# Kernel optimization log

Measured on AMD Instinct MI355X. Metric: run time of the kernel, lower is better.

The kernel has to match this reference:

```python
import jax, jax.numpy as jnp
import numpy as np

B, S, D, H = 2, 2048, 1024, 16
HD = D // H


def setup_inputs() -> dict:
    key = jax.random.key(0)
    ks = jax.random.split(key, 5)
    scale = 1.0 / np.sqrt(D)
    return {
        "query": jax.random.normal(ks[0], (B, S, D), jnp.float32),
        "Wq": jax.random.normal(ks[1], (D, D), jnp.float32) * scale,
        "bq": jnp.zeros((D,), jnp.float32),
        "Wk": jax.random.normal(ks[2], (D, D), jnp.float32) * scale,
        "bk": jnp.zeros((D,), jnp.float32),
        "Wv": jax.random.normal(ks[3], (D, D), jnp.float32) * scale,
        "bv": jnp.zeros((D,), jnp.float32),
        "Wo": jax.random.normal(ks[4], (D, D), jnp.float32) * scale,
        "bo": jnp.zeros((D,), jnp.float32),
    }


def _split_heads(x):
    # [B, S, D] -> [B, H, S, HD]
    return x.reshape(B, S, H, HD).transpose(0, 2, 1, 3)


def reference(query, Wq, bq, Wk, bk, Wv, bv, Wo, bo):
    # Linear projections (torch Linear: x @ W.T + b)
    q = _split_heads(query @ Wq.T + bq)
    k = _split_heads(query @ Wk.T + bk)  # key defaults to query
    v = _split_heads(query @ Wv.T + bv)  # value defaults to query

    # scaled dot-product attention, scores [B, H, S, S]
    scores = jnp.einsum("bhqd,bhkd->bhqk", q, k) / jnp.sqrt(jnp.float32(HD))
    attn = jax.nn.softmax(scores, axis=-1)
    ctx = jnp.einsum("bhqk,bhkd->bhqd", attn, v)

    # combine heads -> [B, S, D]
    ctx = ctx.transpose(0, 2, 1, 3).reshape(B, S, D)
    out = ctx @ Wo.T + bo
    avg_attn = attn.mean(axis=1)  # [B, S, S]
    return out, avg_attn
```

## Files before the change

kernel.cpp:

```cpp
#include <hip/hip_runtime.h>
#include <hip/hip_bf16.h>

#define BB 2
#define SS 2048
#define DD 1024
#define HH 16
#define HDD 64

typedef __bf16 bf16;
typedef bf16 bf16x8 __attribute__((ext_vector_type(8)));
typedef bf16 bf16x4 __attribute__((ext_vector_type(4)));
typedef float f32x4 __attribute__((ext_vector_type(4)));

typedef const __attribute__((address_space(1))) void* gptr_t;
typedef __attribute__((address_space(3))) void* lptr_t;
#define GLL(gp, lp) __builtin_amdgcn_global_load_lds((gptr_t)(gp), (lptr_t)(lp), 16, 0, 0)

__global__ void cast_bf16_k(const float* __restrict__ src, bf16* __restrict__ dst, int n) {
    int i = (blockIdx.x * blockDim.x + threadIdx.x) * 4;
    if (i < n) {
        const float4 f = *(const float4*)(src + i);
        bf16x4 o;
        o[0] = (bf16)f.x; o[1] = (bf16)f.y; o[2] = (bf16)f.z; o[3] = (bf16)f.w;
        *(bf16x4*)(dst + i) = o;
    }
}

template<int MODE>
__global__ __launch_bounds__(256) void gemm_bt(
    const bf16* __restrict__ A, const bf16* __restrict__ Wbase,
    const float* __restrict__ bias0, const float* __restrict__ bias1,
    const float* __restrict__ bias2, void* __restrict__ outp)
{
    __shared__ alignas(16) bf16 As[2][128 * 32];
    __shared__ alignas(16) bf16 Bs[2][128 * 32];

    const int tid  = threadIdx.x;
    const int lane = tid & 63;
    const int wave = tid >> 6;
    const int wr = wave >> 1, wc = wave & 1;
    const int l15 = lane & 15, g = lane >> 4;
    const int m0 = blockIdx.x * 128, n0 = blockIdx.y * 128;
    const int z = blockIdx.z;
    const bf16* W = Wbase + (size_t)z * (DD * DD);
    const float* bias = (MODE == 0) ? (z == 0 ? bias0 : (z == 1 ? bias1 : bias2)) : bias0;

    const int sr = lane >> 2, sc = (lane & 3) * 8;

#define STAGE(buf, kt) {                                                              \
        const int k0 = (kt) * 32;                                                     \
        _Pragma("unroll")                                                             \
        for (int i = 0; i < 2; ++i) {                                                 \
            const int c = wave * 2 + i;                                               \
            GLL(A + (size_t)(m0 + c * 16 + sr) * DD + k0 + sc, &As[buf][c * 512]);    \
            GLL(W + (size_t)(n0 + c * 16 + sr) * DD + k0 + sc, &Bs[buf][c * 512]);    \
        }                                                                             \
    }

    f32x4 acc[4][4];
#pragma unroll
    for (int mi = 0; mi < 4; ++mi)
#pragma unroll
        for (int ni = 0; ni < 4; ++ni) acc[mi][ni] = f32x4{0.f, 0.f, 0.f, 0.f};

    STAGE(0, 0);
    int cur = 0;
    for (int kt = 0; kt < 32; ++kt) {
        __syncthreads();
        if (kt + 1 < 32) STAGE(cur ^ 1, kt + 1);
        bf16x8 af[4], bfr[4];
#pragma unroll
        for (int mi = 0; mi < 4; ++mi)
            af[mi] = *(const bf16x8*)&As[cur][(wr * 64 + mi * 16 + l15) * 32 + g * 8];
#pragma unroll
        for (int ni = 0; ni < 4; ++ni)
            bfr[ni] = *(const bf16x8*)&Bs[cur][(wc * 64 + ni * 16 + l15) * 32 + g * 8];
#pragma unroll
        for (int mi = 0; mi < 4; ++mi)
#pragma unroll
            for (int ni = 0; ni < 4; ++ni)
                acc[mi][ni] = __builtin_amdgcn_mfma_f32_16x16x32_bf16(af[mi], bfr[ni], acc[mi][ni], 0, 0, 0);
        cur ^= 1;
    }
#undef STAGE

    if (MODE == 0) {
        bf16* obase = (bf16*)outp + (size_t)z * (BB * HH * SS * HDD);
#pragma unroll
        for (int mi = 0; mi < 4; ++mi)
#pragma unroll
            for (int ni = 0; ni < 4; ++ni)
#pragma unroll
                for (int r = 0; r < 4; ++r) {
                    const int grow = m0 + wr * 64 + mi * 16 + g * 4 + r;
                    const int gcol = n0 + wc * 64 + ni * 16 + l15;
                    const float val = acc[mi][ni][r] + bias[gcol];
                    const int b = grow >> 11, s = grow & (SS - 1);
                    const int h = gcol >> 6, hd = gcol & 63;
                    obase[((size_t)(b * HH + h) * SS + s) * HDD + hd] = (bf16)val;
                }
    } else {
        float* obase = (float*)outp;
#pragma unroll
        for (int mi = 0; mi < 4; ++mi)
#pragma unroll
            for (int ni = 0; ni < 4; ++ni)
#pragma unroll
                for (int r = 0; r < 4; ++r) {
                    const int grow = m0 + wr * 64 + mi * 16 + g * 4 + r;
                    const int gcol = n0 + wc * 64 + ni * 16 + l15;
                    obase[(size_t)grow * DD + gcol] = acc[mi][ni][r] + bias[gcol];
                }
    }
}

__global__ __launch_bounds__(256) void transpose_v_k(const bf16* __restrict__ src, bf16* __restrict__ dst)
{
    __shared__ bf16 t[64][72];
    const int tid = threadIdx.x;
    const int s0 = blockIdx.x * 64, bh = blockIdx.y;
    {
        const int r = tid >> 3, c8 = (tid & 7) * 8;
#pragma unroll
        for (int i = 0; i < 2; ++i) {
            const bf16x8 v = *(const bf16x8*)(src + ((size_t)bh * SS + s0 + r + i * 32) * HDD + c8);
#pragma unroll
            for (int j = 0; j < 8; ++j) t[c8 + j][r + i * 32] = v[j];
        }
    }
    __syncthreads();
    {
        const int hd = tid >> 2, sl = (tid & 3) * 2;
#pragma unroll
        for (int i = 0; i < 2; ++i) {
            const bf16x8 o = *(const bf16x8*)&t[hd][(sl + i) * 8];
            *(bf16x8*)(dst + ((size_t)bh * HDD + hd) * SS + s0 + (sl + i) * 8) = o;
        }
    }
}

__global__ __launch_bounds__(512) void attn_flash(
    const bf16* __restrict__ q, const bf16* __restrict__ k, const bf16* __restrict__ vT,
    bf16* __restrict__ ctx, float* __restrict__ lrow)
{
    __shared__ alignas(16) bf16 Kt[2][64 * 64];
    __shared__ alignas(16) bf16 Vt[2][64 * 64];
    __shared__ alignas(16) bf16 Pl[8][16 * 72];

    const int tid = threadIdx.x, lane = tid & 63, wave = tid >> 6;
    const int qt = blockIdx.x, bh = blockIdx.y;
    const int q0 = qt * 128 + wave * 16;
    const size_t base = (size_t)bh * SS * HDD;
    const int l15 = lane & 15, g = lane >> 4;

    const bf16* qp = q + base + (size_t)(q0 + l15) * HDD + g * 8;
    const bf16x8 aq0 = *(const bf16x8*)(qp);
    const bf16x8 aq1 = *(const bf16x8*)(qp + 32);

    const int srow_off = lane >> 3, spos = lane & 7;

#define STAGEKV(buf, kv0) {                                                           \
        const int row = wave * 8 + srow_off;                                          \
        const int gs = spos ^ (row & 7);                                              \
        GLL(k  + base + (size_t)((kv0) + row) * HDD + gs * 8, &Kt[buf][wave * 512]);  \
        GLL(vT + base + (size_t)row * SS + (kv0) + gs * 8,    &Vt[buf][wave * 512]);  \
    }

    f32x4 acc[4];
#pragma unroll
    for (int n = 0; n < 4; ++n) acc[n] = f32x4{0.f, 0.f, 0.f, 0.f};
    float lpart[4] = {0.f, 0.f, 0.f, 0.f};

    STAGEKV(0, 0);
    int cur = 0;
    for (int t = 0; t < 32; ++t) {
        __syncthreads();
        if (t + 1 < 32) STAGEKV(cur ^ 1, (t + 1) * 64);

        f32x4 sc[4];
        __builtin_amdgcn_s_setprio(1);
#pragma unroll
        for (int nn = 0; nn < 4; ++nn) {
            const int row = nn * 16 + l15, rx = row & 7;
            const bf16x8 kf0 = *(const bf16x8*)&Kt[cur][row * 64 + ((g    ) ^ rx) * 8];
            const bf16x8 kf1 = *(const bf16x8*)&Kt[cur][row * 64 + ((4 + g) ^ rx) * 8];
            f32x4 c = f32x4{0.f, 0.f, 0.f, 0.f};
            c = __builtin_amdgcn_mfma_f32_16x16x32_bf16(aq0, kf0, c, 0, 0, 0);
            c = __builtin_amdgcn_mfma_f32_16x16x32_bf16(aq1, kf1, c, 0, 0, 0);
            sc[nn] = c * 0.125f;
        }
        __builtin_amdgcn_s_setprio(0);

#pragma unroll
        for (int nn = 0; nn < 4; ++nn)
#pragma unroll
            for (int r = 0; r < 4; ++r) {
                const float p = __expf(sc[nn][r]);
                lpart[r] += p;
                Pl[wave][(g * 4 + r) * 72 + nn * 16 + l15] = (bf16)p;
            }

        const bf16x8 pa0 = *(const bf16x8*)&Pl[wave][l15 * 72 + g * 8];
        const bf16x8 pa1 = *(const bf16x8*)&Pl[wave][l15 * 72 + 32 + g * 8];
        __builtin_amdgcn_s_setprio(1);
#pragma unroll
        for (int n = 0; n < 4; ++n) {
            const int row = n * 16 + l15, rx = row & 7;
            const bf16x8 vf0 = *(const bf16x8*)&Vt[cur][row * 64 + ((g    ) ^ rx) * 8];
            const bf16x8 vf1 = *(const bf16x8*)&Vt[cur][row * 64 + ((4 + g) ^ rx) * 8];
            acc[n] = __builtin_amdgcn_mfma_f32_16x16x32_bf16(pa0, vf0, acc[n], 0, 0, 0);
            acc[n] = __builtin_amdgcn_mfma_f32_16x16x32_bf16(pa1, vf1, acc[n], 0, 0, 0);
        }
        __builtin_amdgcn_s_setprio(0);
        cur ^= 1;
    }
#undef STAGEKV

    const int b = bh >> 4, h = bh & 15;
#pragma unroll
    for (int r = 0; r < 4; ++r) {
        float s = lpart[r];
        s += __shfl_xor(s, 1); s += __shfl_xor(s, 2);
        s += __shfl_xor(s, 4); s += __shfl_xor(s, 8);
        const float inv = 1.0f / s;
        const int srow = q0 + g * 4 + r;
#pragma unroll
        for (int n = 0; n < 4; ++n)
            ctx[(size_t)(b * SS + srow) * DD + h * HDD + n * 16 + l15] = (bf16)(acc[n][r] * inv);
        if (l15 == 0) lrow[(size_t)bh * SS + srow] = s;
    }
}

__global__ __launch_bounds__(512) void avg_attn_k(
    const bf16* __restrict__ q, const bf16* __restrict__ k,
    const float* __restrict__ lrow, float* __restrict__ outAvg)
{
    __shared__ alignas(16) bf16 Ks[2][128 * 64];

    const int tid = threadIdx.x, lane = tid & 63, wave = tid >> 6;
    const int kt = blockIdx.x, qt = blockIdx.y, b = blockIdx.z;
    const int l15 = lane & 15, g = lane >> 4;
    const int qrow0 = qt * 128 + wave * 16;
    const int k0 = kt * 128;

    const int srow_off = lane >> 3, spos = lane & 7;

#define STAGEK(buf, h) {                                                              \
        const size_t hb = ((size_t)(b * HH + (h))) * SS * HDD;                        \
        _Pragma("unroll")                                                             \
        for (int i = 0; i < 2; ++i) {                                                 \
            const int c = wave * 2 + i;                                               \
            const int row = c * 8 + srow_off;                                         \
            const int gs = spos ^ (row & 7);                                          \
            GLL(k + hb + (size_t)(k0 + row) * HDD + gs * 8, &Ks[buf][c * 512]);       \
        }                                                                             \
    }

    f32x4 avg[8];
#pragma unroll
    for (int nn = 0; nn < 8; ++nn) avg[nn] = f32x4{0.f, 0.f, 0.f, 0.f};

    STAGEK(0, 0);
    int cur = 0;
    for (int h = 0; h < HH; ++h) {
        const size_t hb = ((size_t)(b * HH + h)) * SS * HDD;
        const bf16* qp = q + hb + (size_t)(qrow0 + l15) * HDD + g * 8;
        const bf16x8 aq0 = *(const bf16x8*)(qp);
        const bf16x8 aq1 = *(const bf16x8*)(qp + 32);
        float il[4];
#pragma unroll
        for (int r = 0; r < 4; ++r)
            il[r] = 1.0f / lrow[(size_t)(b * HH + h) * SS + qrow0 + g * 4 + r];

        __syncthreads();
        if (h + 1 < HH) STAGEK(cur ^ 1, h + 1);

#pragma unroll
        for (int nn = 0; nn < 8; ++nn) {
            const int row = nn * 16 + l15, rx = row & 7;
            const bf16x8 kf0 = *(const bf16x8*)&Ks[cur][row * 64 + ((g    ) ^ rx) * 8];
            const bf16x8 kf1 = *(const bf16x8*)&Ks[cur][row * 64 + ((4 + g) ^ rx) * 8];
            f32x4 c = f32x4{0.f, 0.f, 0.f, 0.f};
            c = __builtin_amdgcn_mfma_f32_16x16x32_bf16(aq0, kf0, c, 0, 0, 0);
            c = __builtin_amdgcn_mfma_f32_16x16x32_bf16(aq1, kf1, c, 0, 0, 0);
#pragma unroll
            for (int r = 0; r < 4; ++r)
                avg[nn][r] += __expf(c[r] * 0.125f) * il[r];
        }
        cur ^= 1;
    }
#undef STAGEK

#pragma unroll
    for (int nn = 0; nn < 8; ++nn)
#pragma unroll
        for (int r = 0; r < 4; ++r) {
            const int row = qrow0 + g * 4 + r;
            const int col = k0 + nn * 16 + l15;
            outAvg[(size_t)b * SS * SS + (size_t)row * SS + col] = avg[nn][r] * 0.0625f;
        }
}

extern "C" void kernel_launch(void* const* d_in, const int* in_sizes, int n_in,
                              void* d_out, int out_size, void* d_ws, size_t ws_size,
                              hipStream_t stream)
{
    const float* query = (const float*)d_in[0];
    const float* Wq = (const float*)d_in[1];
    const float* bq = (const float*)d_in[2];
    const float* Wk = (const float*)d_in[3];
    const float* bk = (const float*)d_in[4];
    const float* Wv = (const float*)d_in[5];
    const float* bv = (const float*)d_in[6];
    const float* Wo = (const float*)d_in[7];
    const float* bo = (const float*)d_in[8];

    char* ws = (char*)d_ws;
    bf16* qx   = (bf16*)(ws + 0);
    bf16* vT   = (bf16*)(ws + 0);
    bf16* Wqkv = (bf16*)(ws + 8388608);
    bf16* Wob  = (bf16*)(ws + 14680064);
    bf16* qh   = (bf16*)(ws + 16777216);
    bf16* kh   = (bf16*)(ws + 25165824);
    bf16* vh   = (bf16*)(ws + 33554432);
    bf16* ctxb = (bf16*)(ws + 41943040);
    float* lrow = (float*)(ws + 50331648);

    cast_bf16_k<<<4096, 256, 0, stream>>>(query, qx, BB * SS * DD);
    cast_bf16_k<<<1024, 256, 0, stream>>>(Wq, Wqkv,               DD * DD);
    cast_bf16_k<<<1024, 256, 0, stream>>>(Wk, Wqkv + DD * DD,     DD * DD);
    cast_bf16_k<<<1024, 256, 0, stream>>>(Wv, Wqkv + 2 * DD * DD, DD * DD);
    cast_bf16_k<<<1024, 256, 0, stream>>>(Wo, Wob,                DD * DD);

    gemm_bt<0><<<dim3(32, 8, 3), 256, 0, stream>>>(qx, Wqkv, bq, bk, bv, (void*)qh);
    transpose_v_k<<<dim3(32, 32), 256, 0, stream>>>(vh, vT);
    attn_flash<<<dim3(16, 32), 512, 0, stream>>>(qh, kh, vT, ctxb, lrow);
    avg_attn_k<<<dim3(16, 16, 2), 512, 0, stream>>>(qh, kh, lrow, (float*)d_out + (size_t)BB * SS * DD);
    gemm_bt<1><<<dim3(32, 8, 1), 256, 0, stream>>>(ctxb, Wob, bo, bo, bo, d_out);
}
```

Baseline: 265.3 us.

## Fold softmax scale into Q projection, use exp2, merge weight casts, remap attention grid

The Q projection output is pre-multiplied by log2(e)/8, so the attention and avg-attn kernels can call exp2f directly and skip the per-score multiply. The four weight-cast launches become one kernel over a 2D grid, and Wo is written right after Wqkv in the workspace (14680064 bytes = 7·2^21 = 3.5M bf16 elements, so the same region Wob pointed to). The flash-attention grid is flattened to 1D with a remap so consecutive blocks spread across heads, meant to improve cache and XCD locality. Rounding Q to bf16 after scaling slightly changes numerics.

```diff
diff --git a/kernel.cpp b/kernel.cpp
--- a/kernel.cpp
+++ b/kernel.cpp
@@ -6,6 +6,8 @@
 #define DD 1024
 #define HH 16
 #define HDD 64
+
+#define QSCALE 0.1803368867f
 
 typedef __bf16 bf16;
 typedef bf16 bf16x8 __attribute__((ext_vector_type(8)));
@@ -24,6 +26,19 @@
         o[0] = (bf16)f.x; o[1] = (bf16)f.y; o[2] = (bf16)f.z; o[3] = (bf16)f.w;
         *(bf16x4*)(dst + i) = o;
     }
+}
+
+__global__ void cast_w4_k(const float* __restrict__ w0, const float* __restrict__ w1,
+                          const float* __restrict__ w2, const float* __restrict__ w3,
+                          bf16* __restrict__ dst) {
+    const int z = blockIdx.y;
+    const float* s = (z == 0) ? w0 : (z == 1) ? w1 : (z == 2) ? w2 : w3;
+    bf16* d = dst + (size_t)z * (DD * DD);
+    int i = (blockIdx.x * blockDim.x + threadIdx.x) * 4;
+    const float4 f = *(const float4*)(s + i);
+    bf16x4 o;
+    o[0] = (bf16)f.x; o[1] = (bf16)f.y; o[2] = (bf16)f.z; o[3] = (bf16)f.w;
+    *(bf16x4*)(d + i) = o;
 }
 
 template<int MODE>
@@ -44,6 +59,7 @@
     const int z = blockIdx.z;
     const bf16* W = Wbase + (size_t)z * (DD * DD);
     const float* bias = (MODE == 0) ? (z == 0 ? bias0 : (z == 1 ? bias1 : bias2)) : bias0;
+    const float oscale = (MODE == 0 && z == 0) ? QSCALE : 1.0f;
 
     const int sr = lane >> 2, sc = (lane & 3) * 8;
 
@@ -94,7 +110,7 @@
                 for (int r = 0; r < 4; ++r) {
                     const int grow = m0 + wr * 64 + mi * 16 + g * 4 + r;
                     const int gcol = n0 + wc * 64 + ni * 16 + l15;
-                    const float val = acc[mi][ni][r] + bias[gcol];
+                    const float val = (acc[mi][ni][r] + bias[gcol]) * oscale;
                     const int b = grow >> 11, s = grow & (SS - 1);
                     const int h = gcol >> 6, hd = gcol & 63;
                     obase[((size_t)(b * HH + h) * SS + s) * HDD + hd] = (bf16)val;
@@ -148,7 +164,9 @@
     __shared__ alignas(16) bf16 Pl[8][16 * 72];
 
     const int tid = threadIdx.x, lane = tid & 63, wave = tid >> 6;
-    const int qt = blockIdx.x, bh = blockIdx.y;
+    const int d = blockIdx.x;
+    const int bh = (d & 7) * 4 + ((d >> 3) & 3);
+    const int qt = d >> 5;
     const int q0 = qt * 128 + wave * 16;
     const size_t base = (size_t)bh * SS * HDD;
     const int l15 = lane & 15, g = lane >> 4;
@@ -187,7 +205,7 @@
             f32x4 c = f32x4{0.f, 0.f, 0.f, 0.f};
             c = __builtin_amdgcn_mfma_f32_16x16x32_bf16(aq0, kf0, c, 0, 0, 0);
             c = __builtin_amdgcn_mfma_f32_16x16x32_bf16(aq1, kf1, c, 0, 0, 0);
-            sc[nn] = c * 0.125f;
+            sc[nn] = c;
         }
         __builtin_amdgcn_s_setprio(0);
 
@@ -195,7 +213,7 @@
         for (int nn = 0; nn < 4; ++nn)
 #pragma unroll
             for (int r = 0; r < 4; ++r) {
-                const float p = __expf(sc[nn][r]);
+                const float p = exp2f(sc[nn][r]);
                 lpart[r] += p;
                 Pl[wave][(g * 4 + r) * 72 + nn * 16 + l15] = (bf16)p;
             }
@@ -285,7 +303,7 @@
             c = __builtin_amdgcn_mfma_f32_16x16x32_bf16(aq1, kf1, c, 0, 0, 0);
 #pragma unroll
             for (int r = 0; r < 4; ++r)
-                avg[nn][r] += __expf(c[r] * 0.125f) * il[r];
+                avg[nn][r] += exp2f(c[r]) * il[r];
         }
         cur ^= 1;
     }
@@ -327,14 +345,12 @@
     float* lrow = (float*)(ws + 50331648);
 
     cast_bf16_k<<<4096, 256, 0, stream>>>(query, qx, BB * SS * DD);
-    cast_bf16_k<<<1024, 256, 0, stream>>>(Wq, Wqkv,               DD * DD);
-    cast_bf16_k<<<1024, 256, 0, stream>>>(Wk, Wqkv + DD * DD,     DD * DD);
-    cast_bf16_k<<<1024, 256, 0, stream>>>(Wv, Wqkv + 2 * DD * DD, DD * DD);
-    cast_bf16_k<<<1024, 256, 0, stream>>>(Wo, Wob,                DD * DD);
+    cast_w4_k<<<dim3(1024, 4), 256, 0, stream>>>(Wq, Wk, Wv, Wo, Wqkv);
+    (void)Wob;
 
     gemm_bt<0><<<dim3(32, 8, 3), 256, 0, stream>>>(qx, Wqkv, bq, bk, bv, (void*)qh);
     transpose_v_k<<<dim3(32, 32), 256, 0, stream>>>(vh, vT);
-    attn_flash<<<dim3(16, 32), 512, 0, stream>>>(qh, kh, vT, ctxb, lrow);
+    attn_flash<<<512, 512, 0, stream>>>(qh, kh, vT, ctxb, lrow);
     avg_attn_k<<<dim3(16, 16, 2), 512, 0, stream>>>(qh, kh, lrow, (float*)d_out + (size_t)BB * SS * DD);
-    gemm_bt<1><<<dim3(32, 8, 1), 256, 0, stream>>>(ctxb, Wob, bo, bo, bo, d_out);
-}
+    gemm_bt<1><<<dim3(32, 8, 1), 256, 0, stream>>>(ctxb, Wqkv + (size_t)3 * DD * DD, bo, bo, bo, d_out);
+}
```

Measured after the change: 278.1 us. +4.8%, slower.
